# Kernel optimization log

Hardware: AMD Instinct MI355X
Metric: run time of the kernel (lower is better)

The kernel has to match this reference:

```python
import jax, jax.numpy as jnp
import numpy as np

COUNT, L1, L2, L3 = 8, 3072, 15, 32


def setup_inputs() -> dict:
    key = jax.random.key(0)
    ks = jax.random.split(key, 10)
    B = 16384
    x = jax.random.uniform(ks[0], (B, L1), dtype=jnp.float32)
    ls_indices = jax.random.randint(ks[1], (B,), 0, COUNT, dtype=jnp.int32)
    s = 1.0 / np.sqrt(L1)
    l1_w = jax.random.uniform(ks[2], (COUNT * (L2 + 1), L1), minval=-s, maxval=s, dtype=jnp.float32)
    l1_b = jax.random.uniform(ks[3], (COUNT * (L2 + 1),), minval=-s, maxval=s, dtype=jnp.float32)
    # l1_fact initialized to zero in the module; use small random values for a
    # meaningful numeric test (same math either way)
    l1f_w = 0.01 * jax.random.normal(ks[4], (L2 + 1, L1), dtype=jnp.float32)
    l1f_b = 0.01 * jax.random.normal(ks[5], (L2 + 1,), dtype=jnp.float32)
    s2 = 1.0 / np.sqrt(2 * L2)
    l2_w = jax.random.uniform(ks[6], (COUNT * L3, 2 * L2), minval=-s2, maxval=s2, dtype=jnp.float32)
    l2_b = jax.random.uniform(ks[7], (COUNT * L3,), minval=-s2, maxval=s2, dtype=jnp.float32)
    s3 = 1.0 / np.sqrt(L3)
    out_w = jax.random.uniform(ks[8], (COUNT, L3), minval=-s3, maxval=s3, dtype=jnp.float32)
    out_b = jnp.zeros((COUNT,), dtype=jnp.float32)
    return {"x": x, "ls_indices": ls_indices, "l1_w": l1_w, "l1_b": l1_b,
            "l1f_w": l1f_w, "l1f_b": l1f_b, "l2_w": l2_w, "l2_b": l2_b,
            "out_w": out_w, "out_b": out_b}


def _gather_bucket(dense, idx):
    # dense: [B, count, F]; idx: [B] -> [B, F]
    return jnp.take_along_axis(dense, idx[:, None, None], axis=1)[:, 0, :]


def reference(x, ls_indices, l1_w, l1_b, l1f_w, l1f_b, l2_w, l2_b, out_w, out_b):
    B = x.shape[0]
    idx = ls_indices.reshape(-1)
    # L1 stage: dense over all buckets, then gather selected bucket
    l1s = (x @ l1_w.T + l1_b).reshape(B, COUNT, L2 + 1)
    l1c = _gather_bucket(l1s, idx)                      # [B, L2+1]
    l1f = x @ l1f_w.T + l1f_b                           # [B, L2+1]
    l1c_main, l1c_out = l1c[:, :L2], l1c[:, L2:]
    l1f_main, l1f_out = l1f[:, :L2], l1f[:, L2:]
    l1x = l1c_main + l1f_main
    # squared-clipped-ReLU pair: [x^2 * 127/128, x] clamped to [0,1]
    l1x = jnp.clip(jnp.concatenate([jnp.square(l1x) * (127.0 / 128.0), l1x], axis=1), 0.0, 1.0)
    # L2 stage
    l2s = (l1x @ l2_w.T + l2_b).reshape(B, COUNT, L3)
    l2x = jnp.clip(_gather_bucket(l2s, idx), 0.0, 1.0)  # [B, L3]
    # output stage
    l3s = (l2x @ out_w.T + out_b).reshape(B, COUNT, 1)
    l3c = _gather_bucket(l3s, idx)                      # [B, 1]
    return l3c + l1f_out + l1c_out
```

## Files before the change

kernel.cpp:

```cpp
#include <hip/hip_runtime.h>
#include <stdint.h>

#define CNT 8
#define L1D 3072
#define NB 16384
#define BM 32
#define BN 128
#define BK 64
#define KITERS (L1D / BK)
#define LSTR 72

typedef float  float4v  __attribute__((ext_vector_type(4)));
typedef short  short8   __attribute__((ext_vector_type(8)));
typedef unsigned short ushort4v __attribute__((ext_vector_type(4)));

__device__ __forceinline__ unsigned short f2bf(float f) {
  uint32_t u = __builtin_bit_cast(uint32_t, f);
  u += 0x7fffu + ((u >> 16) & 1u);
  return (unsigned short)(u >> 16);
}

__global__ void prep_kernel(const float* __restrict__ l1w, const float* __restrict__ l1b,
                            const float* __restrict__ l1fw, const float* __restrict__ l1fb,
                            unsigned short* __restrict__ cw, float* __restrict__ cb) {
  const int n = blockIdx.y;
  const int k = blockIdx.x * 256 + threadIdx.x;
  cw[n * L1D + k] = f2bf(l1w[n * L1D + k] + l1fw[(n & 15) * L1D + k]);
  if (blockIdx.x == 0 && n == 0 && threadIdx.x < 128)
    cb[threadIdx.x] = l1b[threadIdx.x] + l1fb[threadIdx.x & 15];
}

union __align__(16) SMem {
  struct {
    unsigned short A[2][BM * LSTR];
    unsigned short B[2][BN * LSTR];
  } st;
  struct {
    float yg[BM][20];
    float l2w[960 * 9];
    float outw[256];
    float l2b[256];
    float bias[128];
    int   buck[BM];
  } ep;
};

__global__ __launch_bounds__(256, 2) void fused_kernel(
    const float* __restrict__ x, const int* __restrict__ lsi,
    const unsigned short* __restrict__ cw, const float* __restrict__ cb,
    const float* __restrict__ gl2w, const float* __restrict__ gl2b,
    const float* __restrict__ goutw, const float* __restrict__ goutb,
    float* __restrict__ out) {
  __shared__ SMem sm;
  const int tid  = threadIdx.x;
  const int lane = tid & 63;
  const int wid  = tid >> 6;
  const int mw   = wid & 1;
  const int nw   = wid >> 1;
  const int rowbase = blockIdx.x * BM;

  const int ar = tid >> 4, af = tid & 15;
  const int br = tid >> 3, bc = tid & 7;
  const float* xp = x + (size_t)(rowbase + ar) * L1D + af * 4;
  const unsigned short* wp = cw + (size_t)br * L1D + bc * 8;

  float4v aR[2];
  short8  bR[4];
  float4v acc[4];
#pragma unroll
  for (int j = 0; j < 4; ++j) acc[j] = float4v{0.f, 0.f, 0.f, 0.f};

#pragma unroll
  for (int p = 0; p < 2; ++p) aR[p] = *(const float4v*)(xp + (size_t)p * 16 * L1D);
#pragma unroll
  for (int p = 0; p < 4; ++p) bR[p] = *(const short8*)(wp + (size_t)p * 32 * L1D);
#pragma unroll
  for (int p = 0; p < 2; ++p) {
    ushort4v v = {f2bf(aR[p].x), f2bf(aR[p].y), f2bf(aR[p].z), f2bf(aR[p].w)};
    *(ushort4v*)&sm.st.A[0][(p * 16 + ar) * LSTR + af * 4] = v;
  }
#pragma unroll
  for (int p = 0; p < 4; ++p)
    *(short8*)&sm.st.B[0][(p * 32 + br) * LSTR + bc * 8] = bR[p];
  __syncthreads();

  for (int it = 0; it < KITERS; ++it) {
    const int buf = it & 1;
    if (it + 1 < KITERS) {
      const int koff = (it + 1) * BK;
#pragma unroll
      for (int p = 0; p < 2; ++p) aR[p] = *(const float4v*)(xp + (size_t)p * 16 * L1D + koff);
#pragma unroll
      for (int p = 0; p < 4; ++p) bR[p] = *(const short8*)(wp + (size_t)p * 32 * L1D + koff);
    }
#pragma unroll
    for (int ks = 0; ks < 2; ++ks) {
      const int kk = ks * 32 + (lane >> 4) * 8;
      short8 afr, bfr[4];
      afr = *(const short8*)&sm.st.A[buf][(mw * 16 + (lane & 15)) * LSTR + kk];
#pragma unroll
      for (int j = 0; j < 4; ++j)
        bfr[j] = *(const short8*)&sm.st.B[buf][((4 * nw + j) * 16 + (lane & 15)) * LSTR + kk];
#pragma unroll
      for (int j = 0; j < 4; ++j)
        acc[j] = __builtin_amdgcn_mfma_f32_16x16x32_bf16(afr, bfr[j], acc[j], 0, 0, 0);
    }
    if (it + 1 < KITERS) {
#pragma unroll
      for (int p = 0; p < 2; ++p) {
        ushort4v v = {f2bf(aR[p].x), f2bf(aR[p].y), f2bf(aR[p].z), f2bf(aR[p].w)};
        *(ushort4v*)&sm.st.A[buf ^ 1][(p * 16 + ar) * LSTR + af * 4] = v;
      }
#pragma unroll
      for (int p = 0; p < 4; ++p)
        *(short8*)&sm.st.B[buf ^ 1][(p * 32 + br) * LSTR + bc * 8] = bR[p];
      __syncthreads();
    }
  }
  __syncthreads();

  if (tid < BM)  sm.ep.buck[tid] = lsi[rowbase + tid];
  if (tid < 128) sm.ep.bias[tid] = cb[tid];
  {
    const int b2 = tid >> 5, n2 = tid & 31;
    sm.ep.outw[n2 * 8 + b2] = goutw[tid];
    sm.ep.l2b[tid] = gl2b[tid];
  }
  for (int i = tid; i < 960 * 8; i += 256) {
    const int b = i / 960;
    const int rem = i - b * 960;
    sm.ep.l2w[rem * 9 + b] = gl2w[i];
  }
  __syncthreads();

#pragma unroll
  for (int j = 0; j < 4; ++j) {
    const int nt = 4 * nw + j;
#pragma unroll
    for (int rg = 0; rg < 4; ++rg) {
      const int r = mw * 16 + (lane >> 4) * 4 + rg;
      if (sm.ep.buck[r] == nt) sm.ep.yg[r][lane & 15] = acc[j][rg];
    }
  }
  __syncthreads();

  {
    const int r = tid >> 3, q = tid & 7;
    const int b = sm.ep.buck[r];
    float act[30];
#pragma unroll
    for (int c = 0; c < 15; ++c) {
      const float v = sm.ep.yg[r][c] + sm.ep.bias[b * 16 + c];
      act[c]      = fminf(v * v * (127.0f / 128.0f), 1.0f);
      act[15 + c] = fminf(fmaxf(v, 0.0f), 1.0f);
    }
    const float y15 = sm.ep.yg[r][15] + sm.ep.bias[b * 16 + 15];
    float o = 0.0f;
#pragma unroll
    for (int nn = 0; nn < 4; ++nn) {
      const int n = q * 4 + nn;
      float s = sm.ep.l2b[b * 32 + n];
#pragma unroll
      for (int k = 0; k < 30; ++k) s += act[k] * sm.ep.l2w[(n * 30 + k) * 9 + b];
      s = fminf(fmaxf(s, 0.0f), 1.0f);
      o += s * sm.ep.outw[n * 8 + b];
    }
    o += __shfl_down(o, 4, 8);
    o += __shfl_down(o, 2, 8);
    o += __shfl_down(o, 1, 8);
    if (q == 0) out[rowbase + r] = o + y15 + goutb[b];
  }
}

extern "C" void kernel_launch(void* const* d_in, const int* in_sizes, int n_in,
                              void* d_out, int out_size, void* d_ws, size_t ws_size,
                              hipStream_t stream) {
  const float* x    = (const float*)d_in[0];
  const int*   lsi  = (const int*)d_in[1];
  const float* l1w  = (const float*)d_in[2];
  const float* l1b  = (const float*)d_in[3];
  const float* l1fw = (const float*)d_in[4];
  const float* l1fb = (const float*)d_in[5];
  const float* l2w  = (const float*)d_in[6];
  const float* l2b  = (const float*)d_in[7];
  const float* outw = (const float*)d_in[8];
  const float* outb = (const float*)d_in[9];
  float* out = (float*)d_out;

  unsigned short* cw = (unsigned short*)d_ws;
  float* cb = (float*)((char*)d_ws + 128 * L1D * sizeof(unsigned short));

  prep_kernel<<<dim3(12, 128), 256, 0, stream>>>(l1w, l1b, l1fw, l1fb, cw, cb);
  fused_kernel<<<NB / BM, 256, 0, stream>>>(x, lsi, cw, cb, l2w, l2b, outw, outb, out);
}
```

Baseline: 314.8 us.

## Sort rows by bucket and compute only the selected bucket's L1 outputs

Adds a prep-stage bucket sort: one block counts rows per bucket and builds a padded permutation plus a chunk-to-bucket descriptor table. The main kernel then handles 16 same-bucket rows per block, computing only that bucket's 16 L1 outputs instead of all 128, with K split across four waves and summed in shared memory. This removes 8x redundant MFMA work and the epilogue gather, but x rows are now read in gathered order straight from global memory without LDS staging. The single-block sort is serialized and adds a dependency before the main kernel.

```diff
diff --git a/kernel.cpp b/kernel.cpp
--- a/kernel.cpp
+++ b/kernel.cpp
@@ -1,18 +1,14 @@
 #include <hip/hip_runtime.h>
 #include <stdint.h>
 
-#define CNT 8
 #define L1D 3072
 #define NB 16384
-#define BM 32
-#define BN 128
-#define BK 64
-#define KITERS (L1D / BK)
-#define LSTR 72
+#define CH 16
+#define NCHUNK 1032
+#define PERM_CAP (NCHUNK * CH)
 
-typedef float  float4v  __attribute__((ext_vector_type(4)));
-typedef short  short8   __attribute__((ext_vector_type(8)));
-typedef unsigned short ushort4v __attribute__((ext_vector_type(4)));
+typedef float  float4v __attribute__((ext_vector_type(4)));
+typedef short  short8  __attribute__((ext_vector_type(8)));
 
 __device__ __forceinline__ unsigned short f2bf(float f) {
   uint32_t u = __builtin_bit_cast(uint32_t, f);
@@ -22,153 +18,149 @@
 
 __global__ void prep_kernel(const float* __restrict__ l1w, const float* __restrict__ l1b,
                             const float* __restrict__ l1fw, const float* __restrict__ l1fb,
-                            unsigned short* __restrict__ cw, float* __restrict__ cb) {
-  const int n = blockIdx.y;
-  const int k = blockIdx.x * 256 + threadIdx.x;
-  cw[n * L1D + k] = f2bf(l1w[n * L1D + k] + l1fw[(n & 15) * L1D + k]);
-  if (blockIdx.x == 0 && n == 0 && threadIdx.x < 128)
-    cb[threadIdx.x] = l1b[threadIdx.x] + l1fb[threadIdx.x & 15];
+                            const int* __restrict__ lsi,
+                            unsigned short* __restrict__ cw, float* __restrict__ cb,
+                            int* __restrict__ perm, int* __restrict__ desc) {
+  if (blockIdx.x < 1536) {
+    const int flat = blockIdx.x * 256 + threadIdx.x;
+    const int n = flat / L1D;
+    const int k = flat - n * L1D;
+    cw[flat] = f2bf(l1w[flat] + l1fw[(n & 15) * L1D + k]);
+    if (blockIdx.x == 0 && threadIdx.x < 128)
+      cb[threadIdx.x] = l1b[threadIdx.x] + l1fb[threadIdx.x & 15];
+    return;
+  }
+  __shared__ int cnt[8], base[8], padded[8], pos[8];
+  const int t = threadIdx.x;
+  if (t < 8) cnt[t] = 0;
+  __syncthreads();
+  int loc[8] = {0, 0, 0, 0, 0, 0, 0, 0};
+  for (int i = 0; i < NB / 256; ++i) loc[lsi[i * 256 + t]]++;
+#pragma unroll
+  for (int b = 0; b < 8; ++b) if (loc[b]) atomicAdd(&cnt[b], loc[b]);
+  __syncthreads();
+  if (t == 0) {
+    int off = 0;
+    for (int b = 0; b < 8; ++b) {
+      base[b] = off;
+      padded[b] = (cnt[b] + CH - 1) & ~(CH - 1);
+      off += padded[b];
+    }
+  }
+  __syncthreads();
+  if (t < 8) pos[t] = base[t];
+  for (int i = t; i < PERM_CAP; i += 256) perm[i] = -1;
+  for (int g = t; g < NCHUNK; g += 256) {
+    int d = -1;
+#pragma unroll
+    for (int b = 0; b < 8; ++b) {
+      const int c0 = base[b] / CH, c1 = (base[b] + padded[b]) / CH;
+      if (g >= c0 && g < c1) d = b;
+    }
+    desc[g] = d;
+  }
+  __syncthreads();
+  for (int i = 0; i < NB / 256; ++i) {
+    const int r = i * 256 + t;
+    const int p = atomicAdd(&pos[lsi[r]], 1);
+    perm[p] = r;
+  }
 }
 
-union __align__(16) SMem {
-  struct {
-    unsigned short A[2][BM * LSTR];
-    unsigned short B[2][BN * LSTR];
-  } st;
-  struct {
-    float yg[BM][20];
-    float l2w[960 * 9];
-    float outw[256];
-    float l2b[256];
-    float bias[128];
-    int   buck[BM];
-  } ep;
-};
-
 __global__ __launch_bounds__(256, 2) void fused_kernel(
-    const float* __restrict__ x, const int* __restrict__ lsi,
-    const unsigned short* __restrict__ cw, const float* __restrict__ cb,
+    const float* __restrict__ x, const unsigned short* __restrict__ cw,
+    const float* __restrict__ cb, const int* __restrict__ perm, const int* __restrict__ desc,
     const float* __restrict__ gl2w, const float* __restrict__ gl2b,
     const float* __restrict__ goutw, const float* __restrict__ goutb,
     float* __restrict__ out) {
-  __shared__ SMem sm;
-  const int tid  = threadIdx.x;
+  const int b = desc[blockIdx.x];
+  if (b < 0) return;
+  const int tid = threadIdx.x;
   const int lane = tid & 63;
-  const int wid  = tid >> 6;
-  const int mw   = wid & 1;
-  const int nw   = wid >> 1;
-  const int rowbase = blockIdx.x * BM;
+  const int w = tid >> 6;
+  const int col = lane & 15, quad = lane >> 4;
 
-  const int ar = tid >> 4, af = tid & 15;
-  const int br = tid >> 3, bc = tid & 7;
-  const float* xp = x + (size_t)(rowbase + ar) * L1D + af * 4;
-  const unsigned short* wp = cw + (size_t)br * L1D + bc * 8;
+  __shared__ struct {
+    float yg[4][CH][17];
+    float l2w[32][31];
+    float l2b[32], outw[32], bias[16];
+    int   prow[CH];
+  } sm;
 
-  float4v aR[2];
-  short8  bR[4];
-  float4v acc[4];
-#pragma unroll
-  for (int j = 0; j < 4; ++j) acc[j] = float4v{0.f, 0.f, 0.f, 0.f};
+  if (tid < 32) {
+    sm.l2b[tid]  = gl2b[b * 32 + tid];
+    sm.outw[tid] = goutw[b * 32 + tid];
+    if (tid < CH) sm.prow[tid] = perm[blockIdx.x * CH + tid];
+    if (tid < 16) sm.bias[tid] = cb[b * 16 + tid];
+  }
+  for (int i = tid; i < 960; i += 256) {
+    const int n = i / 30, k = i - n * 30;
+    sm.l2w[n][k] = gl2w[(b * 32 + n) * 30 + k];
+  }
+
+  const int ri = perm[blockIdx.x * CH + col];
+  const float* ap = x + (size_t)(ri < 0 ? 0 : ri) * L1D + w * 32 + quad * 8;
+  const unsigned short* bp = cw + (size_t)(b * 16 + col) * L1D + w * 32 + quad * 8;
+
+  float4v acc = {0.f, 0.f, 0.f, 0.f};
+  float4v a0 = *(const float4v*)ap;
+  float4v a1 = *(const float4v*)(ap + 4);
+  short8  bf = *(const short8*)bp;
+#pragma unroll 4
+  for (int it = 0; it < 23; ++it) {
+    const float* apn = ap + (it + 1) * 128;
+    float4v na0 = *(const float4v*)apn;
+    float4v na1 = *(const float4v*)(apn + 4);
+    short8  nbf = *(const short8*)(bp + (it + 1) * 128);
+    short8 af;
+    af[0] = (short)f2bf(a0.x); af[1] = (short)f2bf(a0.y);
+    af[2] = (short)f2bf(a0.z); af[3] = (short)f2bf(a0.w);
+    af[4] = (short)f2bf(a1.x); af[5] = (short)f2bf(a1.y);
+    af[6] = (short)f2bf(a1.z); af[7] = (short)f2bf(a1.w);
+    acc = __builtin_amdgcn_mfma_f32_16x16x32_bf16(af, bf, acc, 0, 0, 0);
+    a0 = na0; a1 = na1; bf = nbf;
+  }
+  {
+    short8 af;
+    af[0] = (short)f2bf(a0.x); af[1] = (short)f2bf(a0.y);
+    af[2] = (short)f2bf(a0.z); af[3] = (short)f2bf(a0.w);
+    af[4] = (short)f2bf(a1.x); af[5] = (short)f2bf(a1.y);
+    af[6] = (short)f2bf(a1.z); af[7] = (short)f2bf(a1.w);
+    acc = __builtin_amdgcn_mfma_f32_16x16x32_bf16(af, bf, acc, 0, 0, 0);
+  }
 
 #pragma unroll
-  for (int p = 0; p < 2; ++p) aR[p] = *(const float4v*)(xp + (size_t)p * 16 * L1D);
-#pragma unroll
-  for (int p = 0; p < 4; ++p) bR[p] = *(const short8*)(wp + (size_t)p * 32 * L1D);
-#pragma unroll
-  for (int p = 0; p < 2; ++p) {
-    ushort4v v = {f2bf(aR[p].x), f2bf(aR[p].y), f2bf(aR[p].z), f2bf(aR[p].w)};
-    *(ushort4v*)&sm.st.A[0][(p * 16 + ar) * LSTR + af * 4] = v;
-  }
-#pragma unroll
-  for (int p = 0; p < 4; ++p)
-    *(short8*)&sm.st.B[0][(p * 32 + br) * LSTR + bc * 8] = bR[p];
-  __syncthreads();
-
-  for (int it = 0; it < KITERS; ++it) {
-    const int buf = it & 1;
-    if (it + 1 < KITERS) {
-      const int koff = (it + 1) * BK;
-#pragma unroll
-      for (int p = 0; p < 2; ++p) aR[p] = *(const float4v*)(xp + (size_t)p * 16 * L1D + koff);
-#pragma unroll
-      for (int p = 0; p < 4; ++p) bR[p] = *(const short8*)(wp + (size_t)p * 32 * L1D + koff);
-    }
-#pragma unroll
-    for (int ks = 0; ks < 2; ++ks) {
-      const int kk = ks * 32 + (lane >> 4) * 8;
-      short8 afr, bfr[4];
-      afr = *(const short8*)&sm.st.A[buf][(mw * 16 + (lane & 15)) * LSTR + kk];
-#pragma unroll
-      for (int j = 0; j < 4; ++j)
-        bfr[j] = *(const short8*)&sm.st.B[buf][((4 * nw + j) * 16 + (lane & 15)) * LSTR + kk];
-#pragma unroll
-      for (int j = 0; j < 4; ++j)
-        acc[j] = __builtin_amdgcn_mfma_f32_16x16x32_bf16(afr, bfr[j], acc[j], 0, 0, 0);
-    }
-    if (it + 1 < KITERS) {
-#pragma unroll
-      for (int p = 0; p < 2; ++p) {
-        ushort4v v = {f2bf(aR[p].x), f2bf(aR[p].y), f2bf(aR[p].z), f2bf(aR[p].w)};
-        *(ushort4v*)&sm.st.A[buf ^ 1][(p * 16 + ar) * LSTR + af * 4] = v;
-      }
-#pragma unroll
-      for (int p = 0; p < 4; ++p)
-        *(short8*)&sm.st.B[buf ^ 1][(p * 32 + br) * LSTR + bc * 8] = bR[p];
-      __syncthreads();
-    }
-  }
-  __syncthreads();
-
-  if (tid < BM)  sm.ep.buck[tid] = lsi[rowbase + tid];
-  if (tid < 128) sm.ep.bias[tid] = cb[tid];
-  {
-    const int b2 = tid >> 5, n2 = tid & 31;
-    sm.ep.outw[n2 * 8 + b2] = goutw[tid];
-    sm.ep.l2b[tid] = gl2b[tid];
-  }
-  for (int i = tid; i < 960 * 8; i += 256) {
-    const int b = i / 960;
-    const int rem = i - b * 960;
-    sm.ep.l2w[rem * 9 + b] = gl2w[i];
-  }
-  __syncthreads();
-
-#pragma unroll
-  for (int j = 0; j < 4; ++j) {
-    const int nt = 4 * nw + j;
-#pragma unroll
-    for (int rg = 0; rg < 4; ++rg) {
-      const int r = mw * 16 + (lane >> 4) * 4 + rg;
-      if (sm.ep.buck[r] == nt) sm.ep.yg[r][lane & 15] = acc[j][rg];
-    }
-  }
+  for (int rg = 0; rg < 4; ++rg) sm.yg[w][quad * 4 + rg][col] = acc[rg];
   __syncthreads();
 
   {
-    const int r = tid >> 3, q = tid & 7;
-    const int b = sm.ep.buck[r];
+    const int r = tid >> 4, q = tid & 15;
+    const int rr = sm.prow[r];
     float act[30];
 #pragma unroll
     for (int c = 0; c < 15; ++c) {
-      const float v = sm.ep.yg[r][c] + sm.ep.bias[b * 16 + c];
+      const float v = sm.yg[0][r][c] + sm.yg[1][r][c] + sm.yg[2][r][c] + sm.yg[3][r][c]
+                      + sm.bias[c];
       act[c]      = fminf(v * v * (127.0f / 128.0f), 1.0f);
       act[15 + c] = fminf(fmaxf(v, 0.0f), 1.0f);
     }
-    const float y15 = sm.ep.yg[r][15] + sm.ep.bias[b * 16 + 15];
+    const float y15 = sm.yg[0][r][15] + sm.yg[1][r][15] + sm.yg[2][r][15] + sm.yg[3][r][15]
+                      + sm.bias[15];
     float o = 0.0f;
 #pragma unroll
-    for (int nn = 0; nn < 4; ++nn) {
-      const int n = q * 4 + nn;
-      float s = sm.ep.l2b[b * 32 + n];
+    for (int nn = 0; nn < 2; ++nn) {
+      const int n = q * 2 + nn;
+      float s = sm.l2b[n];
 #pragma unroll
-      for (int k = 0; k < 30; ++k) s += act[k] * sm.ep.l2w[(n * 30 + k) * 9 + b];
+      for (int k = 0; k < 30; ++k) s += act[k] * sm.l2w[n][k];
       s = fminf(fmaxf(s, 0.0f), 1.0f);
-      o += s * sm.ep.outw[n * 8 + b];
+      o += s * sm.outw[n];
     }
-    o += __shfl_down(o, 4, 8);
-    o += __shfl_down(o, 2, 8);
-    o += __shfl_down(o, 1, 8);
-    if (q == 0) out[rowbase + r] = o + y15 + goutb[b];
+    o += __shfl_down(o, 8, 16);
+    o += __shfl_down(o, 4, 16);
+    o += __shfl_down(o, 2, 16);
+    o += __shfl_down(o, 1, 16);
+    if (q == 0 && rr >= 0) out[rr] = o + y15 + goutb[b];
   }
 }
 
@@ -188,8 +180,10 @@
   float* out = (float*)d_out;
 
   unsigned short* cw = (unsigned short*)d_ws;
-  float* cb = (float*)((char*)d_ws + 128 * L1D * sizeof(unsigned short));
+  float* cb  = (float*)((char*)d_ws + 786432);
+  int*   perm = (int*)((char*)d_ws + 786944);
+  int*   desc = (int*)((char*)d_ws + 786944 + PERM_CAP * 4);
 
-  prep_kernel<<<dim3(12, 128), 256, 0, stream>>>(l1w, l1b, l1fw, l1fb, cw, cb);
-  fused_kernel<<<NB / BM, 256, 0, stream>>>(x, lsi, cw, cb, l2w, l2b, outw, outb, out);
+  prep_kernel<<<1537, 256, 0, stream>>>(l1w, l1b, l1fw, l1fb, lsi, cw, cb, perm, desc);
+  fused_kernel<<<NCHUNK, 256, 0, stream>>>(x, cw, cb, perm, desc, l2w, l2b, outw, outb, out);
 }
```

After: 338.8 us. 1.08x slower.
